# Optimization experiments

Hardware: AMD Instinct MI355X
Metric: run time of the kernel (lower is better)

Reference implementation:

```python
import jax, jax.numpy as jnp
import numpy as np

N = 50000
E = 1600000
IN_DIM = 128
OUT_DIM = 128
HEADS = 4
C = OUT_DIM // HEADS  # per-head channels = 32
EDGE_DIM = 16
NEG_SLOPE = 0.2
LN_EPS = 1e-5


def setup_inputs() -> dict:
    key = jax.random.key(0)
    ks = jax.random.split(key, 12)
    s = 1.0 / np.sqrt(IN_DIM)
    return {
        "x": jax.random.normal(ks[0], (N, IN_DIM), dtype=jnp.float32),
        "edge_index": jax.random.randint(ks[1], (2, E), 0, N, dtype=jnp.int64),
        "edge_attr": jax.random.normal(ks[2], (E, EDGE_DIM), dtype=jnp.float32),
        # GATv2Conv params
        "W_l": jax.random.normal(ks[3], (IN_DIM, HEADS * C), dtype=jnp.float32) * s,
        "b_l": jnp.zeros((HEADS * C,), dtype=jnp.float32),
        "W_r": jax.random.normal(ks[4], (IN_DIM, HEADS * C), dtype=jnp.float32) * s,
        "b_r": jnp.zeros((HEADS * C,), dtype=jnp.float32),
        "W_e": jax.random.normal(ks[5], (EDGE_DIM, HEADS * C), dtype=jnp.float32) * (1.0 / np.sqrt(EDGE_DIM)),
        "att": jax.random.normal(ks[6], (HEADS, C), dtype=jnp.float32) * (1.0 / np.sqrt(C)),
        "conv_bias": jnp.zeros((HEADS * C,), dtype=jnp.float32),
        # LayerNorm params
        "gamma": jnp.ones((OUT_DIM,), dtype=jnp.float32),
        "beta": jnp.zeros((OUT_DIM,), dtype=jnp.float32),
    }


def _gat_layer(x, edge_index, edge_attr, W_l, b_l, W_r, b_r, W_e, att, conv_bias, gamma, beta):
    src, dst = edge_index[0], edge_index[1]
    # linear projections -> [N, H, C] / [E, H, C]
    x_l = (x @ W_l + b_l).reshape(N, HEADS, C)  # source-side
    x_r = (x @ W_r + b_r).reshape(N, HEADS, C)  # target-side
    e_f = (edge_attr @ W_e).reshape(E, HEADS, C)
    # GATv2 attention logits per edge/head
    z = x_l[src] + x_r[dst] + e_f                      # [E, H, C]
    z = jnp.where(z >= 0, z, NEG_SLOPE * z)            # LeakyReLU(0.2)
    logits = jnp.einsum('ehc,hc->eh', z, att)          # [E, H]
    # segment softmax over incoming edges of each target node
    m = jax.ops.segment_max(logits, dst, num_segments=N)          # [N, H]
    m = jnp.where(jnp.isfinite(m), m, 0.0)
    ex = jnp.exp(logits - m[dst])                                  # [E, H]
    denom = jax.ops.segment_sum(ex, dst, num_segments=N)          # [N, H]
    alpha = ex / (denom[dst] + 1e-16)                              # [E, H]
    # weighted message aggregation (dropout on alpha skipped: eval mode)
    msg = x_l[src] * alpha[:, :, None]                             # [E, H, C]
    out = jax.ops.segment_sum(msg, dst, num_segments=N)           # [N, H, C]
    out = out.reshape(N, HEADS * C) + conv_bias                    # concat heads
    # LayerNorm -> ReLU -> (dropout: identity) -> residual (Identity since in==out)
    mu = jnp.mean(out, axis=-1, keepdims=True)
    var = jnp.mean(jnp.square(out - mu), axis=-1, keepdims=True)
    out = (out - mu) * jax.lax.rsqrt(var + LN_EPS) * gamma + beta
    out = jax.nn.relu(out)
    return out + x


def reference(x, edge_index, edge_attr, W_l, b_l, W_r, b_r, W_e, att, conv_bias, gamma, beta):
    return _gat_layer(x, edge_index, edge_attr, W_l, b_l, W_r, b_r, W_e, att, conv_bias, gamma, beta)
```

## Files before the change

kernel.cpp:

```cpp
#include <hip/hip_runtime.h>
#include <hip/hip_bf16.h>

#define NPB 16
#define PAD 80
#define OVF_CAP 4096

typedef float f32x2 __attribute__((ext_vector_type(2)));

__device__ __forceinline__ float b2f(__hip_bfloat16 v) { return __bfloat162float(v); }
__device__ __forceinline__ float ldf(const void* p, long i, int f32) {
    return f32 ? ((const float*)p)[i] : b2f(((const __hip_bfloat16*)p)[i]);
}
__device__ __forceinline__ float bflo(unsigned u) { union { unsigned i; float f; } v; v.i = u << 16; return v.f; }
__device__ __forceinline__ float bfhi(unsigned u) { union { unsigned i; float f; } v; v.i = u & 0xffff0000u; return v.f; }
__device__ __forceinline__ float2 ldf2(const void* p, long i2, int f32) {
    if (f32) return ((const float2*)p)[i2];
    unsigned u = ((const unsigned*)p)[i2];
    return make_float2(bflo(u), bfhi(u));
}
__device__ __forceinline__ int ldi(const int* p, long i, int i32) {
    return i32 ? p[i] : p[2 * i];
}
__device__ __forceinline__ int rfl(int v) { return __builtin_amdgcn_readfirstlane(v); }

template <int CTRL>
__device__ __forceinline__ float dpp_add(float v) {
    int s = __builtin_amdgcn_update_dpp(0, __float_as_int(v), CTRL, 0xF, 0xF, true);
    return v + __int_as_float(s);
}

__global__ void zero_i(int* __restrict__ a, long n, int* __restrict__ dt)
{
    long i = (long)blockIdx.x * 256 + threadIdx.x;
    long stride = (long)gridDim.x * 256;
    for (; i < n; i += stride) a[i] = 0;
    if (blockIdx.x == 0 && threadIdx.x == 0 && dt) { dt[0] = 0; dt[1] = 0; }
}

__global__ void fail_stamp(float* __restrict__ out, float code)
{
    if (threadIdx.x == 0 && blockIdx.x == 0) out[0] = code;
}

__global__ void detect_kernel(const void* __restrict__ x, const int* __restrict__ ei,
                              int* __restrict__ dt, int E_)
{
    int t = threadIdx.x;
    const unsigned short* xb = (const unsigned short*)x;
    int f32 = 0;
    for (int i = t; i < 4096; i += 256) {
        int ex = (xb[i] >> 7) & 0xFF;
        if (ex > 140) f32 = 1;
    }
    if (f32) atomicOr(&dt[0], 1);
    int nz = 0;
    for (int i = t; i < 2048; i += 256) nz |= ei[2 * i + 1];
    if (nz) atomicOr(&dt[1], 1);
}

__global__ __launch_bounds__(128) void gemm_scatter(
    const void* __restrict__ x,
    const void* __restrict__ Wl, const void* __restrict__ bl,
    const void* __restrict__ Wr, const void* __restrict__ br,
    const int* __restrict__ ei, const int* __restrict__ dt,
    __hip_bfloat16* __restrict__ xl, __hip_bfloat16* __restrict__ xr,
    int* __restrict__ cnt, int* __restrict__ ovfcnt,
    int2* __restrict__ se_pad, int4* __restrict__ ovf,
    int n, int E_)
{
    __shared__ float xs[NPB][128];
    int t = threadIdx.x;
    int f32 = dt[0], i32 = dt[1];

    long eb = (long)blockIdx.x * 512;
    int sA[4], dA[4], kA[4], eA[4];
#pragma unroll
    for (int i = 0; i < 4; ++i) {
        long e = eb + i * 128 + t;
        int s = -1, d = -1;
        if (e < E_) {
            s = ldi(ei, e, i32);
            d = ldi(ei, E_ + e, i32);
            if (!((unsigned)s < (unsigned)n && (unsigned)d < (unsigned)n)) d = -1;
        }
        sA[i] = s; dA[i] = d; eA[i] = (int)e;
    }
#pragma unroll
    for (int i = 0; i < 4; ++i)
        kA[i] = (dA[i] >= 0) ? atomicAdd(&cnt[dA[i]], 1) : 0;

    int n0 = blockIdx.x * NPB;
    if (n0 < n) {
        for (int j = 0; j < NPB; ++j) {
            int node = n0 + j;
            xs[j][t] = (node < n) ? ldf(x, (long)node * 128 + t, f32) : 0.f;
        }
        __syncthreads();
        f32x2 acc[NPB];
#pragma unroll
        for (int j = 0; j < NPB; ++j) acc[j] = (f32x2){0.f, 0.f};
        for (int k = 0; k < 128; ++k) {
            f32x2 wlr = { ldf(Wl, k * 128 + t, f32), ldf(Wr, k * 128 + t, f32) };
#pragma unroll
            for (int j = 0; j < NPB; ++j) {
                f32x2 xv = { xs[j][k], xs[j][k] };
                acc[j] = __builtin_elementwise_fma(xv, wlr, acc[j]);
            }
        }
        float blv = ldf(bl, t, f32);
        float brv = ldf(br, t, f32);
        for (int j = 0; j < NPB; ++j) {
            int node = n0 + j;
            if (node < n) {
                xl[(long)node * 128 + t] = __float2bfloat16(acc[j].x + blv);
                xr[(long)node * 128 + t] = __float2bfloat16(acc[j].y + brv);
            }
        }
    }

#pragma unroll
    for (int i = 0; i < 4; ++i) {
        if (dA[i] < 0) continue;
        if (kA[i] < PAD) {
            se_pad[(long)dA[i] * PAD + kA[i]] = make_int2(sA[i], eA[i]);
        } else {
            int o = atomicAdd(ovfcnt, 1);
            if (o < OVF_CAP) ovf[o] = make_int4(dA[i], sA[i], eA[i], 0);
        }
    }
}

__global__ __launch_bounds__(256, 4) void node_fused(
    const int* __restrict__ cnt, const int2* __restrict__ se_pad,
    const int4* __restrict__ ovf, const int* __restrict__ ovfcnt,
    const void* __restrict__ ea, const void* __restrict__ We, const void* __restrict__ att,
    const __hip_bfloat16* __restrict__ xl, const __hip_bfloat16* __restrict__ xr,
    const void* __restrict__ cb, const void* __restrict__ gamma,
    const void* __restrict__ beta, const void* __restrict__ x,
    const int* __restrict__ dt, float* __restrict__ out, int N_)
{
    int w = threadIdx.x >> 6, j = threadIdx.x & 63;
    int f32 = dt[0];
    int h = j >> 4;

    f32x2 We2[16];
#pragma unroll
    for (int k = 0; k < 16; ++k) {
        float2 v = ldf2(We, (long)k * 64 + j, f32);
        We2[k] = (f32x2){v.x, v.y};
    }
    float2 attv = ldf2(att, j, f32);
    float2 cbv  = ldf2(cb, j, f32);
    float2 gv   = ldf2(gamma, j, f32);
    float2 bv   = ldf2(beta, j, f32);

    const unsigned* xlu = (const unsigned*)xl;
    const unsigned* xru = (const unsigned*)xr;

    auto edge_ex = [&](const float* a, float x0, float x1, float w0, float w1) -> float {
        f32x2 z = { x0 + w0, x1 + w1 };
#pragma unroll
        for (int k = 0; k < 16; ++k) {
            f32x2 ab = { a[k], a[k] };
            z = __builtin_elementwise_fma(ab, We2[k], z);
        }
        z = __builtin_elementwise_max(z, z * 0.2f);
        float v = fmaf(z.y, attv.y, z.x * attv.x);
        v = dpp_add<0xB1>(v);  v = dpp_add<0x4E>(v);
        v = dpp_add<0x124>(v); v = dpp_add<0x128>(v);
        return __expf(v);
    };

    for (int q = 0; q < 4; ++q) {
        int n = (blockIdx.x * 4 + w) * 4 + q;
        if (n >= N_) break;
        int deg = cnt[n];
        int m = deg < PAD ? deg : PAD;
        long base = (long)n * PAD;
        unsigned urow = xru[(long)n * 64 + j];
        float w0 = bflo(urow), w1 = bfhi(urow);
        f32x2 acc = {0.f, 0.f};
        float den = 0.f;

        if (m > 0) {
            if (f32) {
                int2 se = se_pad[base];
                int sC = rfl(se.x), eC = rfl(se.y);
                unsigned uC = xlu[((long)sC << 6) + j];
                const float4* er = (const float4*)ea + (long)eC * 4;
                float4 r0 = er[0], r1 = er[1], r2 = er[2], r3 = er[3];
                for (int k = 0; k < m; ++k) {
                    int kp = (k + 1 < m) ? k + 1 : 0;
                    int2 seN = se_pad[base + kp];
                    int sN = rfl(seN.x), eN = rfl(seN.y);
                    unsigned uN = xlu[((long)sN << 6) + j];
                    const float4* ern = (const float4*)ea + (long)eN * 4;
                    float4 m0 = ern[0], m1 = ern[1], m2 = ern[2], m3 = ern[3];
                    float a[16] = { r0.x, r0.y, r0.z, r0.w, r1.x, r1.y, r1.z, r1.w,
                                    r2.x, r2.y, r2.z, r2.w, r3.x, r3.y, r3.z, r3.w };
                    float x0 = bflo(uC), x1 = bfhi(uC);
                    float ex = edge_ex(a, x0, x1, w0, w1);
                    acc = __builtin_elementwise_fma((f32x2){ex, ex}, (f32x2){x0, x1}, acc);
                    den += ex;
                    uC = uN; r0 = m0; r1 = m1; r2 = m2; r3 = m3;
                }
            } else {
                int2 se = se_pad[base];
                int sC = rfl(se.x), eC = rfl(se.y);
                unsigned uC = xlu[((long)sC << 6) + j];
                const uint4* er = (const uint4*)ea + (long)eC * 2;
                uint4 b0 = er[0], b1 = er[1];
                for (int k = 0; k < m; ++k) {
                    int kp = (k + 1 < m) ? k + 1 : 0;
                    int2 seN = se_pad[base + kp];
                    int sN = rfl(seN.x), eN = rfl(seN.y);
                    unsigned uN = xlu[((long)sN << 6) + j];
                    const uint4* ern = (const uint4*)ea + (long)eN * 2;
                    uint4 c0 = ern[0], c1 = ern[1];
                    float a[16] = { bflo(b0.x), bfhi(b0.x), bflo(b0.y), bfhi(b0.y),
                                    bflo(b0.z), bfhi(b0.z), bflo(b0.w), bfhi(b0.w),
                                    bflo(b1.x), bfhi(b1.x), bflo(b1.y), bfhi(b1.y),
                                    bflo(b1.z), bfhi(b1.z), bflo(b1.w), bfhi(b1.w) };
                    float x0 = bflo(uC), x1 = bfhi(uC);
                    float ex = edge_ex(a, x0, x1, w0, w1);
                    acc = __builtin_elementwise_fma((f32x2){ex, ex}, (f32x2){x0, x1}, acc);
                    den += ex;
                    uC = uN; b0 = c0; b1 = c1;
                }
            }
        }
        if (deg > PAD) {
            int oc = *ovfcnt; if (oc > OVF_CAP) oc = OVF_CAP;
            for (int o = 0; o < oc; ++o) {
                int4 v4 = ovf[o];
                if (rfl(v4.x) != n) continue;
                int sO = rfl(v4.y), eO = rfl(v4.z);
                unsigned uO = xlu[((long)sO << 6) + j];
                float a[16];
                if (f32) {
                    const float4* er = (const float4*)ea + (long)eO * 4;
                    float4 r0 = er[0], r1 = er[1], r2 = er[2], r3 = er[3];
                    float tmp[16] = { r0.x, r0.y, r0.z, r0.w, r1.x, r1.y, r1.z, r1.w,
                                      r2.x, r2.y, r2.z, r2.w, r3.x, r3.y, r3.z, r3.w };
#pragma unroll
                    for (int k = 0; k < 16; ++k) a[k] = tmp[k];
                } else {
                    const uint4* er = (const uint4*)ea + (long)eO * 2;
                    uint4 b0 = er[0], b1 = er[1];
                    float tmp[16] = { bflo(b0.x), bfhi(b0.x), bflo(b0.y), bfhi(b0.y),
                                      bflo(b0.z), bfhi(b0.z), bflo(b0.w), bfhi(b0.w),
                                      bflo(b1.x), bfhi(b1.x), bflo(b1.y), bfhi(b1.y),
                                      bflo(b1.z), bfhi(b1.z), bflo(b1.w), bfhi(b1.w) };
#pragma unroll
                    for (int k = 0; k < 16; ++k) a[k] = tmp[k];
                }
                float x0 = bflo(uO), x1 = bfhi(uO);
                float ex = edge_ex(a, x0, x1, w0, w1);
                acc = __builtin_elementwise_fma((f32x2){ex, ex}, (f32x2){x0, x1}, acc);
                den += ex;
            }
        }

        float rden = 1.f / (den + 1e-16f);
        float o0 = acc.x * rden + cbv.x;
        float o1 = acc.y * rden + cbv.y;

        float s = o0 + o1;
#pragma unroll
        for (int o = 1; o < 64; o <<= 1) s += __shfl_xor(s, o, 64);
        float mu = s * (1.f / 128.f);
        float d0 = o0 - mu, d1 = o1 - mu;
        float vs = d0 * d0 + d1 * d1;
#pragma unroll
        for (int o = 1; o < 64; o <<= 1) vs += __shfl_xor(vs, o, 64);
        float rs = rsqrtf(vs * (1.f / 128.f) + 1e-5f);
        float2 xv = ldf2(x, (long)n * 64 + j, f32);
        float y0 = fmaxf(d0 * rs * gv.x + bv.x, 0.f) + xv.x;
        float y1 = fmaxf(d1 * rs * gv.y + bv.y, 0.f) + xv.y;
        *(float2*)(out + (long)n * 128 + 2 * j) = make_float2(y0, y1);
    }
}

extern "C" void kernel_launch(void* const* d_in, const int* in_sizes, int n_in,
                              void* d_out, int out_size, void* d_ws, size_t ws_size,
                              hipStream_t stream) {
    const void* x     = d_in[0];
    const int*  ei    = (const int*)d_in[1];
    const void* ea    = d_in[2];
    const void* Wl    = d_in[3];
    const void* bl    = d_in[4];
    const void* Wr    = d_in[5];
    const void* br    = d_in[6];
    const void* We    = d_in[7];
    const void* att   = d_in[8];
    const void* cb    = d_in[9];
    const void* gamma = d_in[10];
    const void* beta  = d_in[11];
    float* out = (float*)d_out;

    const int N_ = in_sizes[0] / 128;
    const int E_ = in_sizes[2] / 16;

    size_t need = 0;
    auto sz = [&](size_t b) { size_t r = need; need += (b + 255) & ~(size_t)255; return r; };
    size_t o_xl   = sz((size_t)N_ * 128 * 2);
    size_t o_xr   = sz((size_t)N_ * 128 * 2);
    size_t o_cnt  = sz((size_t)(N_ + 8) * 4);
    size_t o_dt   = sz(256);
    size_t o_se   = sz((size_t)N_ * PAD * 8);
    size_t o_ovf  = sz((size_t)OVF_CAP * 16);

    if (need > ws_size) {
        fail_stamp<<<1, 64, 0, stream>>>(out, 16384.f);
        return;
    }
    char* p = (char*)d_ws;
    __hip_bfloat16* xl   = (__hip_bfloat16*)(p + o_xl);
    __hip_bfloat16* xr   = (__hip_bfloat16*)(p + o_xr);
    int*   cnt           = (int*)(p + o_cnt);
    int*   ovfcnt        = cnt + N_;
    int*   dt            = (int*)(p + o_dt);
    int2*  se_pad        = (int2*)(p + o_se);
    int4*  ovf           = (int4*)(p + o_ovf);

    zero_i<<<256, 256, 0, stream>>>(cnt, N_ + 8, dt);
    detect_kernel<<<1, 256, 0, stream>>>(x, ei, dt, E_);
    int gGemm = (N_ + NPB - 1) / NPB;
    int gScat = (E_ + 511) / 512;
    int grid0 = gGemm > gScat ? gGemm : gScat;
    gemm_scatter<<<grid0, 128, 0, stream>>>(x, Wl, bl, Wr, br, ei, dt, xl, xr,
                                            cnt, ovfcnt, se_pad, ovf, N_, E_);
    node_fused<<<(N_ + 15) / 16, 256, 0, stream>>>(cnt, se_pad, ovf, ovfcnt, ea, We, att,
                                                   xl, xr, cb, gamma, beta, x, dt, out, N_);
}
```

Baseline: 633.9 us.

## Pre-gather edge attributes as bf16 into dst-sorted padded buffer

The scatter kernel now reads each edge's 16 attribute floats, packs them to bf16, and writes them next to the source index in a destination-ordered padded slot array. The node kernel then streams edge attributes contiguously instead of doing a random gather per edge. PAD drops to 64, NPB rises to 32, and the launch-bounds occupancy hint changes. The cost is an extra random read and a 32-byte write per edge in the scatter pass, bf16 rounding of edge attributes, and more overflow edges for high-degree nodes.

```diff
diff --git a/kernel.cpp b/kernel.cpp
--- a/kernel.cpp
+++ b/kernel.cpp
@@ -1,8 +1,8 @@
 #include <hip/hip_runtime.h>
 #include <hip/hip_bf16.h>
 
-#define NPB 16
-#define PAD 80
+#define NPB 32
+#define PAD 64
 #define OVF_CAP 4096
 
 typedef float f32x2 __attribute__((ext_vector_type(2)));
@@ -22,6 +22,11 @@
     return i32 ? p[i] : p[2 * i];
 }
 __device__ __forceinline__ int rfl(int v) { return __builtin_amdgcn_readfirstlane(v); }
+__device__ __forceinline__ unsigned pk2(float a, float b) {
+    __hip_bfloat16 ha = __float2bfloat16(a), hb = __float2bfloat16(b);
+    unsigned short ua = *(unsigned short*)&ha, ub = *(unsigned short*)&hb;
+    return (unsigned)ua | ((unsigned)ub << 16);
+}
 
 template <int CTRL>
 __device__ __forceinline__ float dpp_add(float v) {
@@ -62,10 +67,11 @@
     const void* __restrict__ x,
     const void* __restrict__ Wl, const void* __restrict__ bl,
     const void* __restrict__ Wr, const void* __restrict__ br,
+    const void* __restrict__ ea,
     const int* __restrict__ ei, const int* __restrict__ dt,
     __hip_bfloat16* __restrict__ xl, __hip_bfloat16* __restrict__ xr,
     int* __restrict__ cnt, int* __restrict__ ovfcnt,
-    int2* __restrict__ se_pad, int4* __restrict__ ovf,
+    int* __restrict__ src_pad, uint4* __restrict__ ea_pad, int4* __restrict__ ovf,
     int n, int E_)
 {
     __shared__ float xs[NPB][128];
@@ -74,6 +80,7 @@
 
     long eb = (long)blockIdx.x * 512;
     int sA[4], dA[4], kA[4], eA[4];
+    uint4 eaR0[4], eaR1[4];
 #pragma unroll
     for (int i = 0; i < 4; ++i) {
         long e = eb + i * 128 + t;
@@ -88,6 +95,23 @@
 #pragma unroll
     for (int i = 0; i < 4; ++i)
         kA[i] = (dA[i] >= 0) ? atomicAdd(&cnt[dA[i]], 1) : 0;
+#pragma unroll
+    for (int i = 0; i < 4; ++i) {
+        eaR0[i] = make_uint4(0u, 0u, 0u, 0u); eaR1[i] = eaR0[i];
+        if (dA[i] < 0) continue;
+        long e = eA[i];
+        if (f32) {
+            const float4* q = (const float4*)ea + e * 4;
+            float4 q0 = q[0], q1 = q[1], q2 = q[2], q3 = q[3];
+            eaR0[i] = make_uint4(pk2(q0.x, q0.y), pk2(q0.z, q0.w),
+                                 pk2(q1.x, q1.y), pk2(q1.z, q1.w));
+            eaR1[i] = make_uint4(pk2(q2.x, q2.y), pk2(q2.z, q2.w),
+                                 pk2(q3.x, q3.y), pk2(q3.z, q3.w));
+        } else {
+            const uint4* q = (const uint4*)ea + e * 2;
+            eaR0[i] = q[0]; eaR1[i] = q[1];
+        }
+    }
 
     int n0 = blockIdx.x * NPB;
     if (n0 < n) {
@@ -122,7 +146,10 @@
     for (int i = 0; i < 4; ++i) {
         if (dA[i] < 0) continue;
         if (kA[i] < PAD) {
-            se_pad[(long)dA[i] * PAD + kA[i]] = make_int2(sA[i], eA[i]);
+            long slot = (long)dA[i] * PAD + kA[i];
+            src_pad[slot] = sA[i];
+            ea_pad[2 * slot]     = eaR0[i];
+            ea_pad[2 * slot + 1] = eaR1[i];
         } else {
             int o = atomicAdd(ovfcnt, 1);
             if (o < OVF_CAP) ovf[o] = make_int4(dA[i], sA[i], eA[i], 0);
@@ -130,8 +157,38 @@
     }
 }
 
-__global__ __launch_bounds__(256, 4) void node_fused(
-    const int* __restrict__ cnt, const int2* __restrict__ se_pad,
+#define EDGE_COMPUTE(E0, E1, UC)                                                       \
+    {                                                                                  \
+        f32x2 z = { bflo(UC) + w0, bfhi(UC) + w1 };                                    \
+        z = __builtin_elementwise_fma((f32x2){bflo(E0.x), bflo(E0.x)}, W[0],  z);      \
+        z = __builtin_elementwise_fma((f32x2){bfhi(E0.x), bfhi(E0.x)}, W[1],  z);      \
+        z = __builtin_elementwise_fma((f32x2){bflo(E0.y), bflo(E0.y)}, W[2],  z);      \
+        z = __builtin_elementwise_fma((f32x2){bfhi(E0.y), bfhi(E0.y)}, W[3],  z);      \
+        z = __builtin_elementwise_fma((f32x2){bflo(E0.z), bflo(E0.z)}, W[4],  z);      \
+        z = __builtin_elementwise_fma((f32x2){bfhi(E0.z), bfhi(E0.z)}, W[5],  z);      \
+        z = __builtin_elementwise_fma((f32x2){bflo(E0.w), bflo(E0.w)}, W[6],  z);      \
+        z = __builtin_elementwise_fma((f32x2){bfhi(E0.w), bfhi(E0.w)}, W[7],  z);      \
+        z = __builtin_elementwise_fma((f32x2){bflo(E1.x), bflo(E1.x)}, W[8],  z);      \
+        z = __builtin_elementwise_fma((f32x2){bfhi(E1.x), bfhi(E1.x)}, W[9],  z);      \
+        z = __builtin_elementwise_fma((f32x2){bflo(E1.y), bflo(E1.y)}, W[10], z);      \
+        z = __builtin_elementwise_fma((f32x2){bfhi(E1.y), bfhi(E1.y)}, W[11], z);      \
+        z = __builtin_elementwise_fma((f32x2){bflo(E1.z), bflo(E1.z)}, W[12], z);      \
+        z = __builtin_elementwise_fma((f32x2){bfhi(E1.z), bfhi(E1.z)}, W[13], z);      \
+        z = __builtin_elementwise_fma((f32x2){bflo(E1.w), bflo(E1.w)}, W[14], z);      \
+        z = __builtin_elementwise_fma((f32x2){bfhi(E1.w), bfhi(E1.w)}, W[15], z);      \
+        z = __builtin_elementwise_max(z, z * 0.2f);                \
+        float vv = fmaf(z.y, attv.y, z.x * attv.x);                                    \
+        vv = dpp_add<0xB1>(vv);  vv = dpp_add<0x4E>(vv);                               \
+        vv = dpp_add<0x124>(vv); vv = dpp_add<0x128>(vv);        \
+        float exv = __expf(vv);                                                        \
+        acc = __builtin_elementwise_fma((f32x2){exv, exv},                             \
+                                        (f32x2){bflo(UC), bfhi(UC)}, acc);             \
+        den += exv;                                                                    \
+    }
+
+__global__ __launch_bounds__(256, 2) void node_fused(
+    const int* __restrict__ cnt, const int* __restrict__ src_pad,
+    const uint4* __restrict__ ea_pad,
     const int4* __restrict__ ovf, const int* __restrict__ ovfcnt,
     const void* __restrict__ ea, const void* __restrict__ We, const void* __restrict__ att,
     const __hip_bfloat16* __restrict__ xl, const __hip_bfloat16* __restrict__ xr,
@@ -141,13 +198,12 @@
 {
     int w = threadIdx.x >> 6, j = threadIdx.x & 63;
     int f32 = dt[0];
-    int h = j >> 4;
-
-    f32x2 We2[16];
+
+    f32x2 W[16];
 #pragma unroll
     for (int k = 0; k < 16; ++k) {
         float2 v = ldf2(We, (long)k * 64 + j, f32);
-        We2[k] = (f32x2){v.x, v.y};
+        W[k] = (f32x2){v.x, v.y};
     }
     float2 attv = ldf2(att, j, f32);
     float2 cbv  = ldf2(cb, j, f32);
@@ -156,20 +212,6 @@
 
     const unsigned* xlu = (const unsigned*)xl;
     const unsigned* xru = (const unsigned*)xr;
-
-    auto edge_ex = [&](const float* a, float x0, float x1, float w0, float w1) -> float {
-        f32x2 z = { x0 + w0, x1 + w1 };
-#pragma unroll
-        for (int k = 0; k < 16; ++k) {
-            f32x2 ab = { a[k], a[k] };
-            z = __builtin_elementwise_fma(ab, We2[k], z);
-        }
-        z = __builtin_elementwise_max(z, z * 0.2f);
-        float v = fmaf(z.y, attv.y, z.x * attv.x);
-        v = dpp_add<0xB1>(v);  v = dpp_add<0x4E>(v);
-        v = dpp_add<0x124>(v); v = dpp_add<0x128>(v);
-        return __expf(v);
-    };
 
     for (int q = 0; q < 4; ++q) {
         int n = (blockIdx.x * 4 + w) * 4 + q;
@@ -183,50 +225,16 @@
         float den = 0.f;
 
         if (m > 0) {
-            if (f32) {
-                int2 se = se_pad[base];
-                int sC = rfl(se.x), eC = rfl(se.y);
-                unsigned uC = xlu[((long)sC << 6) + j];
-                const float4* er = (const float4*)ea + (long)eC * 4;
-                float4 r0 = er[0], r1 = er[1], r2 = er[2], r3 = er[3];
-                for (int k = 0; k < m; ++k) {
-                    int kp = (k + 1 < m) ? k + 1 : 0;
-                    int2 seN = se_pad[base + kp];
-                    int sN = rfl(seN.x), eN = rfl(seN.y);
-                    unsigned uN = xlu[((long)sN << 6) + j];
-                    const float4* ern = (const float4*)ea + (long)eN * 4;
-                    float4 m0 = ern[0], m1 = ern[1], m2 = ern[2], m3 = ern[3];
-                    float a[16] = { r0.x, r0.y, r0.z, r0.w, r1.x, r1.y, r1.z, r1.w,
-                                    r2.x, r2.y, r2.z, r2.w, r3.x, r3.y, r3.z, r3.w };
-                    float x0 = bflo(uC), x1 = bfhi(uC);
-                    float ex = edge_ex(a, x0, x1, w0, w1);
-                    acc = __builtin_elementwise_fma((f32x2){ex, ex}, (f32x2){x0, x1}, acc);
-                    den += ex;
-                    uC = uN; r0 = m0; r1 = m1; r2 = m2; r3 = m3;
-                }
-            } else {
-                int2 se = se_pad[base];
-                int sC = rfl(se.x), eC = rfl(se.y);
-                unsigned uC = xlu[((long)sC << 6) + j];
-                const uint4* er = (const uint4*)ea + (long)eC * 2;
-                uint4 b0 = er[0], b1 = er[1];
-                for (int k = 0; k < m; ++k) {
-                    int kp = (k + 1 < m) ? k + 1 : 0;
-                    int2 seN = se_pad[base + kp];
-                    int sN = rfl(seN.x), eN = rfl(seN.y);
-                    unsigned uN = xlu[((long)sN << 6) + j];
-                    const uint4* ern = (const uint4*)ea + (long)eN * 2;
-                    uint4 c0 = ern[0], c1 = ern[1];
-                    float a[16] = { bflo(b0.x), bfhi(b0.x), bflo(b0.y), bfhi(b0.y),
-                                    bflo(b0.z), bfhi(b0.z), bflo(b0.w), bfhi(b0.w),
-                                    bflo(b1.x), bfhi(b1.x), bflo(b1.y), bfhi(b1.y),
-                                    bflo(b1.z), bfhi(b1.z), bflo(b1.w), bfhi(b1.w) };
-                    float x0 = bflo(uC), x1 = bfhi(uC);
-                    float ex = edge_ex(a, x0, x1, w0, w1);
-                    acc = __builtin_elementwise_fma((f32x2){ex, ex}, (f32x2){x0, x1}, acc);
-                    den += ex;
-                    uC = uN; b0 = c0; b1 = c1;
-                }
+            int sC = rfl(src_pad[base]);
+            uint4 eC0 = ea_pad[2 * base], eC1 = ea_pad[2 * base + 1];
+            unsigned uC = xlu[((long)sC << 6) + j];
+            for (int k = 0; k < m; ++k) {
+                long sl = base + ((k + 1 < m) ? k + 1 : k);
+                int sN = rfl(src_pad[sl]);
+                uint4 eN0 = ea_pad[2 * sl], eN1 = ea_pad[2 * sl + 1];
+                unsigned uN = xlu[((long)sN << 6) + j];
+                EDGE_COMPUTE(eC0, eC1, uC);
+                sC = sN; eC0 = eN0; eC1 = eN1; uC = uN;
             }
         }
         if (deg > PAD) {
@@ -234,30 +242,21 @@
             for (int o = 0; o < oc; ++o) {
                 int4 v4 = ovf[o];
                 if (rfl(v4.x) != n) continue;
-                int sO = rfl(v4.y), eO = rfl(v4.z);
+                int sO = rfl(v4.y); long eO = rfl(v4.z);
                 unsigned uO = xlu[((long)sO << 6) + j];
-                float a[16];
+                uint4 E0, E1;
                 if (f32) {
-                    const float4* er = (const float4*)ea + (long)eO * 4;
-                    float4 r0 = er[0], r1 = er[1], r2 = er[2], r3 = er[3];
-                    float tmp[16] = { r0.x, r0.y, r0.z, r0.w, r1.x, r1.y, r1.z, r1.w,
-                                      r2.x, r2.y, r2.z, r2.w, r3.x, r3.y, r3.z, r3.w };
-#pragma unroll
-                    for (int k = 0; k < 16; ++k) a[k] = tmp[k];
+                    const float4* qr = (const float4*)ea + eO * 4;
+                    float4 q0 = qr[0], q1 = qr[1], q2 = qr[2], q3 = qr[3];
+                    E0 = make_uint4(pk2(q0.x, q0.y), pk2(q0.z, q0.w),
+                                    pk2(q1.x, q1.y), pk2(q1.z, q1.w));
+                    E1 = make_uint4(pk2(q2.x, q2.y), pk2(q2.z, q2.w),
+                                    pk2(q3.x, q3.y), pk2(q3.z, q3.w));
                 } else {
-                    const uint4* er = (const uint4*)ea + (long)eO * 2;
-                    uint4 b0 = er[0], b1 = er[1];
-                    float tmp[16] = { bflo(b0.x), bfhi(b0.x), bflo(b0.y), bfhi(b0.y),
-                                      bflo(b0.z), bfhi(b0.z), bflo(b0.w), bfhi(b0.w),
-                                      bflo(b1.x), bfhi(b1.x), bflo(b1.y), bfhi(b1.y),
-                                      bflo(b1.z), bfhi(b1.z), bflo(b1.w), bfhi(b1.w) };
-#pragma unroll
-                    for (int k = 0; k < 16; ++k) a[k] = tmp[k];
+                    const uint4* qr = (const uint4*)ea + eO * 2;
+                    E0 = qr[0]; E1 = qr[1];
                 }
-                float x0 = bflo(uO), x1 = bfhi(uO);
-                float ex = edge_ex(a, x0, x1, w0, w1);
-                acc = __builtin_elementwise_fma((f32x2){ex, ex}, (f32x2){x0, x1}, acc);
-                den += ex;
+                EDGE_COMPUTE(E0, E1, uO);
             }
         }
 
@@ -307,7 +306,8 @@
     size_t o_xr   = sz((size_t)N_ * 128 * 2);
     size_t o_cnt  = sz((size_t)(N_ + 8) * 4);
     size_t o_dt   = sz(256);
-    size_t o_se   = sz((size_t)N_ * PAD * 8);
+    size_t o_src  = sz((size_t)N_ * PAD * 4);
+    size_t o_eap  = sz((size_t)N_ * PAD * 32);
     size_t o_ovf  = sz((size_t)OVF_CAP * 16);
 
     if (need > ws_size) {
@@ -320,7 +320,8 @@
     int*   cnt           = (int*)(p + o_cnt);
     int*   ovfcnt        = cnt + N_;
     int*   dt            = (int*)(p + o_dt);
-    int2*  se_pad        = (int2*)(p + o_se);
+    int*   src_pad       = (int*)(p + o_src);
+    uint4* ea_pad        = (uint4*)(p + o_eap);
     int4*  ovf           = (int4*)(p + o_ovf);
 
     zero_i<<<256, 256, 0, stream>>>(cnt, N_ + 8, dt);
@@ -328,8 +329,9 @@
     int gGemm = (N_ + NPB - 1) / NPB;
     int gScat = (E_ + 511) / 512;
     int grid0 = gGemm > gScat ? gGemm : gScat;
-    gemm_scatter<<<grid0, 128, 0, stream>>>(x, Wl, bl, Wr, br, ei, dt, xl, xr,
-                                            cnt, ovfcnt, se_pad, ovf, N_, E_);
-    node_fused<<<(N_ + 15) / 16, 256, 0, stream>>>(cnt, se_pad, ovf, ovfcnt, ea, We, att,
-                                                   xl, xr, cb, gamma, beta, x, dt, out, N_);
-}
+    gemm_scatter<<<grid0, 128, 0, stream>>>(x, Wl, bl, Wr, br, ea, ei, dt, xl, xr,
+                                            cnt, ovfcnt, src_pad, ea_pad, ovf, N_, E_);
+    node_fused<<<(N_ + 15) / 16, 256, 0, stream>>>(cnt, src_pad, ea_pad, ovf, ovfcnt,
+                                                   ea, We, att, xl, xr,
+                                                   cb, gamma, beta, x, dt, out, N_);
+}
```

New measurement: 852.3 us. 1.34x slower.
